# Kernel optimization log

Hardware: AMD Instinct MI355X
Metric: run time of the kernel (lower is better)

## Reference

```python
import jax, jax.numpy as jnp
import numpy as np

HIDDEN = 1024
HEADS = 16
HEAD_DIM = HIDDEN // HEADS


def setup_inputs() -> dict:
    key = jax.random.key(0)
    ks = jax.random.split(key, 8)
    B, S = 2, 2048
    scale = 1.0 / np.sqrt(HIDDEN)
    return {
        "hidden_states": jax.random.normal(ks[0], (B, S, HIDDEN), dtype=jnp.float32),
        "attention_mask": jax.random.randint(ks[1], (B, S), 0, 2, dtype=jnp.int32),
        "Wq": jax.random.normal(ks[2], (HIDDEN, HIDDEN), dtype=jnp.float32) * scale,
        "bq": jax.random.normal(ks[3], (HIDDEN,), dtype=jnp.float32) * 0.02,
        "Wk": jax.random.normal(ks[4], (HIDDEN, HIDDEN), dtype=jnp.float32) * scale,
        "bk": jax.random.normal(ks[5], (HIDDEN,), dtype=jnp.float32) * 0.02,
        "Wv": jax.random.normal(ks[6], (HIDDEN, HIDDEN), dtype=jnp.float32) * scale,
        "bv": jax.random.normal(ks[7], (HIDDEN,), dtype=jnp.float32) * 0.02,
    }


def _split_heads(x):
    # [B, S, H*D] -> [B, H, S, D]
    B, S, _ = x.shape
    return x.reshape(B, S, HEADS, HEAD_DIM).transpose(0, 2, 1, 3)


def reference(hidden_states, attention_mask, Wq, bq, Wk, bk, Wv, bv):
    B, S, _ = hidden_states.shape
    q = _split_heads(hidden_states @ Wq + bq) / jnp.sqrt(jnp.asarray(HEAD_DIM, hidden_states.dtype))
    k = _split_heads(hidden_states @ Wk + bk)
    v = _split_heads(hidden_states @ Wv + bv)
    # scores: [B, H, S, S]
    scores = jnp.einsum("bhqd,bhkd->bhqk", q, k).astype(jnp.float32)
    mask = attention_mask[:, None, None, :]  # [B,1,1,S]
    scores = jnp.where(mask == 0, jnp.float32(-1e8), scores)
    probs = jax.nn.softmax(scores, axis=-1).astype(v.dtype)
    ctx = jnp.einsum("bhqk,bhkd->bhqd", probs, v)
    return ctx.transpose(0, 2, 1, 3).reshape(B, S, HIDDEN)
```

## Files before the change

kernel.cpp:

```cpp
#include <hip/hip_runtime.h>
#include <math.h>

typedef __attribute__((ext_vector_type(4))) float f32x4;
typedef __attribute__((ext_vector_type(16))) float f32x16;
typedef _Float16 f16x8 __attribute__((ext_vector_type(8)));
typedef __fp16 fp16x2 __attribute__((ext_vector_type(2)));
typedef unsigned int uintv2 __attribute__((ext_vector_type(2)));

#define MFMA16(a, b, c) __builtin_amdgcn_mfma_f32_16x16x32_f16((a), (b), (c), 0, 0, 0)
#define MFMA32(a, b, c) __builtin_amdgcn_mfma_f32_32x32x16_f16((a), (b), (c), 0, 0, 0)

__device__ __forceinline__ unsigned short f2h(float f) {
    union { _Float16 h; unsigned short u; } v; v.h = (_Float16)f; return v.u;
}
__device__ __forceinline__ unsigned pk2f(float a, float b) {
    union { fp16x2 h; unsigned u; } v; v.h = __builtin_amdgcn_cvt_pkrtz(a, b); return v.u;
}

#if defined(__has_builtin)
#if __has_builtin(__builtin_amdgcn_global_load_lds)
#define HAVE_GLL 1
#endif
#endif

__device__ __forceinline__ void gload16(const void* g, void* lds) {
#ifdef HAVE_GLL
    __builtin_amdgcn_global_load_lds(
        (const __attribute__((address_space(1))) void*)g,
        (__attribute__((address_space(3))) void*)lds, 16, 0, 0);
#else
    *(f16x8*)lds = *(const f16x8*)g;
#endif
}

__global__ __launch_bounds__(256) void prep_kernel(
    const float* __restrict__ X, const float* __restrict__ Wq,
    const float* __restrict__ Wk, const float* __restrict__ Wv,
    const int* __restrict__ mask,
    unsigned short* __restrict__ XF, unsigned short* __restrict__ WT,
    int* __restrict__ sel, int* __restrict__ kept,
    float* __restrict__ cmask_c) {
    __shared__ float T[64][65];
    __shared__ int wsum[4];
    __shared__ int ktot;
    const int bid = blockIdx.x, t = threadIdx.x;
    if (bid < 4096) {
        int i = (bid * 256 + t) * 4;
        float4 v = *reinterpret_cast<const float4*>(X + i);
        ushort4 h;
        h.x = f2h(v.x); h.y = f2h(v.y); h.z = f2h(v.z); h.w = f2h(v.w);
        *reinterpret_cast<ushort4*>(XF + i) = h;
        return;
    }
    if (bid >= 4864) {
        const int b = bid - 4864;
        const int lane = t & 63, wv = t >> 6;
        const int i0 = b * 2048 + t * 8;
        int mv[8];
        {
            int4 ma = *reinterpret_cast<const int4*>(mask + i0);
            int4 mb = *reinterpret_cast<const int4*>(mask + i0 + 4);
            mv[0] = ma.x != 0; mv[1] = ma.y != 0; mv[2] = ma.z != 0; mv[3] = ma.w != 0;
            mv[4] = mb.x != 0; mv[5] = mb.y != 0; mv[6] = mb.z != 0; mv[7] = mb.w != 0;
        }
        int s = 0;
#pragma unroll
        for (int j = 0; j < 8; ++j) s += mv[j];
        int v = s;
#pragma unroll
        for (int off = 1; off < 64; off <<= 1) {
            int o = __shfl_up(v, off);
            if (lane >= off) v += o;
        }
        if (lane == 63) wsum[wv] = v;
        __syncthreads();
        int woff = 0;
        for (int i = 0; i < wv; ++i) woff += wsum[i];
        const int incl = v + woff;
        int p = incl - s;
#pragma unroll
        for (int j = 0; j < 8; ++j) {
            if (mv[j]) sel[b * 2048 + p] = t * 8 + j;
            p += mv[j];
        }
        if (t == 255) { ktot = incl; kept[b] = incl; }
        __syncthreads();
        const int kt = ktot;
#pragma unroll
        for (int j = 0; j < 8; ++j)
            cmask_c[i0 + j] = (t * 8 + j < kt) ? -13.f : -1e9f;
        return;
    }
    const int t2 = bid - 4096;
    const int z = t2 >> 8, rem = t2 & 255;
    const int k0 = (rem & 15) * 64, n0 = (rem >> 4) * 64;
    const float* W = (z == 0) ? Wq : ((z == 1) ? Wk : Wv);
    unsigned short* Wo = WT + (size_t)z * 1024 * 1024;
    for (int i = 0; i < 4; i++) {
        int fid = t + i * 256;
        int rr = fid >> 4, cc = fid & 15;
        float4 v = *reinterpret_cast<const float4*>(W + (size_t)(k0 + rr) * 1024 + n0 + cc * 4);
        T[rr][cc * 4 + 0] = v.x; T[rr][cc * 4 + 1] = v.y;
        T[rr][cc * 4 + 2] = v.z; T[rr][cc * 4 + 3] = v.w;
    }
    __syncthreads();
    for (int i = 0; i < 4; i++) {
        int e = t + i * 256;
        int n = e >> 4, kq = (e & 15) * 4;
        ushort4 h;
        h.x = f2h(T[kq + 0][n]); h.y = f2h(T[kq + 1][n]);
        h.z = f2h(T[kq + 2][n]); h.w = f2h(T[kq + 3][n]);
        size_t o = (size_t)(n0 + n) * 1024 + k0 + kq;
        *reinterpret_cast<ushort4*>(Wo + o) = h;
    }
}

__global__ __launch_bounds__(256) void gather_xc_kernel(
    const unsigned short* __restrict__ XF, const int* __restrict__ sel,
    const int* __restrict__ kept, unsigned short* __restrict__ XC) {
    const int x = blockIdx.x, t = threadIdx.x;
    const int b = x >> 11, j = x & 2047;
    if (j >= kept[b]) return;
    const int s = sel[b * 2048 + j];
    const unsigned short* src = XF + ((size_t)b * 2048 + s) * 1024;
    unsigned short* dst = XC + ((size_t)b * 2048 + j) * 1024;
    *reinterpret_cast<ushort4*>(dst + t * 4) =
        *reinterpret_cast<const ushort4*>(src + t * 4);
}

__global__ __launch_bounds__(256, 3) void qkv_gemm_kernel(
    const unsigned short* __restrict__ XF, const unsigned short* __restrict__ XC,
    const unsigned short* __restrict__ WT,
    const float* __restrict__ bq, const float* __restrict__ bk,
    const float* __restrict__ bv, const int* __restrict__ kept,
    unsigned short* __restrict__ QF, unsigned short* __restrict__ KC,
    unsigned short* __restrict__ VC) {
    __shared__ __align__(16) char smem[3][2][8192];
    const int z = blockIdx.z;
    const unsigned short* Wz = WT + (size_t)z * 1024 * 1024;
    const float* bias = (z == 0) ? bq : ((z == 1) ? bk : bv);
    const int n0 = blockIdx.y * 128;
    int bb = 0, mb0;
    const unsigned short* Xs;
    if (z == 0) {
        mb0 = blockIdx.x * 128;
        Xs = XF;
    } else {
        bb = blockIdx.x >> 4;
        mb0 = (blockIdx.x & 15) * 128;
        const int kneed = (kept[bb] + 63) & ~63;
        if (mb0 >= kneed) return;
        Xs = XC + (size_t)bb * 2048 * 1024;
    }
    const int tid = threadIdx.x, lane = tid & 63, wid = tid >> 6;
    const int wr = wid >> 1, wc = wid & 1;
    const int g = lane >> 4, r16 = lane & 15;

    f32x4 acc[4][4] = {};

#define QSTAGE(BUFI, K0)                                                             \
    {                                                                                \
        _Pragma("unroll")                                                            \
        for (int p = 0; p < 2; ++p) {                                                \
            int row = p * 64 + (tid >> 2);                                           \
            int ec = ((tid & 3) ^ (row & 3)) * 8;                                    \
            size_t xo = (size_t)(mb0 + row) * 1024 + (K0) + ec;                      \
            size_t wo = (size_t)(n0 + row) * 1024 + (K0) + ec;                       \
            gload16(Xs + xo, &smem[(BUFI)][0][0] + p * 4096 + tid * 16);             \
            gload16(Wz + wo, &smem[(BUFI)][1][0] + p * 4096 + tid * 16);             \
        }                                                                            \
    }

    QSTAGE(0, 0);
    QSTAGE(1, 32);
    int bufc = 0, bufs = 2;
    for (int ki = 0; ki < 32; ++ki) {
        if (ki < 31) {
            asm volatile("s_waitcnt vmcnt(4)" ::: "memory");
        } else {
            asm volatile("s_waitcnt vmcnt(0)" ::: "memory");
        }
        __builtin_amdgcn_s_barrier();
        if (ki < 30) QSTAGE(bufs, (ki + 2) * 32);
        const char* bX = &smem[bufc][0][0];
        const char* bW = &smem[bufc][1][0];
        const int sx = (r16 & 3) << 4;

        f16x8 af[4], bf[4];
#pragma unroll
        for (int mi = 0; mi < 4; ++mi)
            af[mi] = *(const f16x8*)(bX + (wr * 64 + mi * 16 + r16) * 64 + ((g << 4) ^ sx));
#pragma unroll
        for (int ni = 0; ni < 4; ++ni)
            bf[ni] = *(const f16x8*)(bW + (wc * 64 + ni * 16 + r16) * 64 + ((g << 4) ^ sx));
        __builtin_amdgcn_s_setprio(1);
#pragma unroll
        for (int mi = 0; mi < 4; ++mi)
#pragma unroll
            for (int ni = 0; ni < 4; ++ni)
                acc[mi][ni] = MFMA16(af[mi], bf[ni], acc[mi][ni]);
        __builtin_amdgcn_s_setprio(0);
        bufc = (bufc == 2) ? 0 : bufc + 1;
        bufs = (bufs == 2) ? 0 : bufs + 1;
    }

#pragma unroll
    for (int mi = 0; mi < 4; ++mi)
#pragma unroll
        for (int ni = 0; ni < 4; ++ni)
#pragma unroll
            for (int r = 0; r < 4; ++r) {
                int m = mb0 + wr * 64 + mi * 16 + g * 4 + r;
                int n = n0 + wc * 64 + ni * 16 + r16;
                float val = acc[mi][ni][r] + bias[n];
                if (z == 0) val *= 0.18033688011112042f;
                int hh = n >> 6, d = n & 63;
                unsigned short hv = f2h(val);
                if (z == 0) {
                    int b = m >> 11, s = m & 2047;
                    QF[((size_t)(b * 16 + hh) * 2048 + s) * 64 + d] = hv;
                } else if (z == 1) {
                    KC[((size_t)(bb * 16 + hh) * 2048 + m) * 64 + d] = hv;
                } else {
                    VC[((size_t)(bb * 16 + hh) * 64 + d) * 2048 + m] = hv;
                }
            }
}

__global__ __launch_bounds__(256, 4) void attn_kernel(
    const unsigned short* __restrict__ QF, const unsigned short* __restrict__ KC,
    const unsigned short* __restrict__ VC, const float* __restrict__ cmask_c,
    const int* __restrict__ kept, float* __restrict__ out) {
    __shared__ __align__(16) char smem[2][2][8192];
    __shared__ __align__(16) float cmlds[2048];
    const int tid = threadIdx.x;
    const int lane = tid & 63, wid = tid >> 6;
    const int hi = lane >> 5, l31 = lane & 31;
    const int bid = blockIdx.x;
    const int wgid = (bid & 7) * 128 + (bid >> 3);
    const int bh = wgid >> 5, qb = wgid & 31;
    const int b = bh >> 4, h = bh & 15;
    const int qh = wid & 1, kh = wid >> 1;
    const size_t base = (size_t)bh * 2048 * 64;
    const unsigned short* KFh = KC + base;
    const unsigned short* VTh = VC + base;
    const int qrow = qb * 64 + qh * 32 + l31;
    const int swz = (l31 & 7) << 4;
    const int kt = kept[b];
    const int nch = (kt + 63) >> 6;

    f16x8 qf[4];
#pragma unroll
    for (int ks = 0; ks < 4; ++ks)
        qf[ks] = *reinterpret_cast<const f16x8*>(QF + base + (size_t)qrow * 64 + ks * 16 + hi * 8);

    const int lr = lane >> 3, c16 = lane & 7;
    const int gce = (c16 ^ lr) << 3;
    const int pl = wid >> 1, half = wid & 1;
    const unsigned short* mys = pl ? VTh : KFh;
    const int rstr = pl ? 2048 : 64;

    f32x16 ctx[2] = {};
    float l_st = 0.f;

#define STAGE(BUFI, K0)                                                              \
    {                                                                                \
        char* dst = &smem[(BUFI)][pl][0] + half * 4096;                              \
        size_t koff = pl ? (size_t)(K0) : (size_t)(K0) * 64;                         \
        _Pragma("unroll")                                                            \
        for (int i = 0; i < 4; ++i) {                                                \
            int r = half * 32 + i * 8 + lr;                                          \
            gload16(mys + koff + (size_t)r * rstr + gce, dst + i * 1024 + lane * 16);\
        }                                                                            \
    }

    STAGE(0, 0);
    {
        float4 c0 = *reinterpret_cast<const float4*>(cmask_c + b * 2048 + tid * 8);
        float4 c1 = *reinterpret_cast<const float4*>(cmask_c + b * 2048 + tid * 8 + 4);
        *reinterpret_cast<float4*>(&cmlds[tid * 8]) = c0;
        *reinterpret_cast<float4*>(&cmlds[tid * 8 + 4]) = c1;
    }

    for (int ch = 0; ch < nch; ++ch) {
        asm volatile("s_waitcnt vmcnt(0) lgkmcnt(0)" ::: "memory");
        __builtin_amdgcn_s_barrier();
        if (ch + 1 < nch) STAGE((ch + 1) & 1, (ch + 1) * 64);
        const int buf = ch & 1;
        const char* bK = &smem[buf][0][0];
        const char* bV = &smem[buf][1][0];
        const int k0s = ch * 64 + kh * 32;

        f32x16 sc;
        {
            const char* rK = bK + (kh * 32 + l31) * 128;
            f32x16 a = {};
            __builtin_amdgcn_s_setprio(1);
#pragma unroll
            for (int ks = 0; ks < 4; ++ks)
                a = MFMA32(*(const f16x8*)(rK + ((ks * 32 + hi * 16) ^ swz)), qf[ks], a);
            __builtin_amdgcn_s_setprio(0);
            sc = a;
        }

        float p[16];
        float psum = 0.f;
#pragma unroll
        for (int G = 0; G < 4; ++G) {
            float4 cv = *reinterpret_cast<const float4*>(&cmlds[k0s + 8 * G + 4 * hi]);
            int bo = G * 4;
            float e0 = __builtin_amdgcn_exp2f(sc[bo + 0] + cv.x);
            float e1 = __builtin_amdgcn_exp2f(sc[bo + 1] + cv.y);
            float e2 = __builtin_amdgcn_exp2f(sc[bo + 2] + cv.z);
            float e3 = __builtin_amdgcn_exp2f(sc[bo + 3] + cv.w);
            p[bo + 0] = e0; p[bo + 1] = e1; p[bo + 2] = e2; p[bo + 3] = e3;
            psum += e0 + e1 + e2 + e3;
        }
        l_st += psum;

        f16x8 pf[2];
        {
            unsigned a0 = pk2f(p[0], p[1]),   a1 = pk2f(p[2], p[3]);
            unsigned b0 = pk2f(p[4], p[5]),   b1 = pk2f(p[6], p[7]);
            unsigned c0 = pk2f(p[8], p[9]),   c1 = pk2f(p[10], p[11]);
            unsigned d0 = pk2f(p[12], p[13]), d1 = pk2f(p[14], p[15]);
            uintv2 r0 = __builtin_amdgcn_permlane32_swap(a0, b0, false, false);
            uintv2 r1 = __builtin_amdgcn_permlane32_swap(a1, b1, false, false);
            uintv2 r2 = __builtin_amdgcn_permlane32_swap(c0, d0, false, false);
            uintv2 r3 = __builtin_amdgcn_permlane32_swap(c1, d1, false, false);
            union { unsigned u[4]; f16x8 v; } f0, f1;
            f0.u[0] = r0[0]; f0.u[1] = r1[0]; f0.u[2] = r0[1]; f0.u[3] = r1[1];
            f1.u[0] = r2[0]; f1.u[1] = r3[0]; f1.u[2] = r2[1]; f1.u[3] = r3[1];
            pf[0] = f0.v; pf[1] = f1.v;
        }

        __builtin_amdgcn_s_setprio(1);
#pragma unroll
        for (int dt = 0; dt < 2; ++dt) {
            const char* rV = bV + (dt * 32 + l31) * 128;
            f32x16 a = ctx[dt];
#pragma unroll
            for (int ks = 0; ks < 2; ++ks)
                a = MFMA32(*(const f16x8*)(rV + ((kh * 64 + ks * 32 + hi * 16) ^ swz)), pf[ks], a);
            ctx[dt] = a;
        }
        __builtin_amdgcn_s_setprio(0);
    }

    l_st += __shfl_xor(l_st, 32);
    asm volatile("s_waitcnt lgkmcnt(0)" ::: "memory");
    __builtin_amdgcn_s_barrier();
    float* scr = (float*)&smem[0][0][0];
    if (kh) {
        float* dst = scr + qh * 2304 + lane * 36;
#pragma unroll
        for (int dt = 0; dt < 2; ++dt)
#pragma unroll
            for (int G = 0; G < 4; ++G) {
                float4 st;
                st.x = ctx[dt][G * 4 + 0]; st.y = ctx[dt][G * 4 + 1];
                st.z = ctx[dt][G * 4 + 2]; st.w = ctx[dt][G * 4 + 3];
                *reinterpret_cast<float4*>(dst + dt * 16 + G * 4) = st;
            }
        scr[4608 + qh * 64 + lane] = l_st;
        asm volatile("s_waitcnt lgkmcnt(0)" ::: "memory");
    }
    __builtin_amdgcn_s_barrier();
    if (!kh) {
        const float* src = scr + qh * 2304 + lane * 36;
        float l_full = l_st + scr[4608 + qh * 64 + lane];
        float inv_l = 1.0f / l_full;
        size_t ob0 = ((size_t)b * 2048 + qrow) * 1024 + h * 64 + 4 * hi;
#pragma unroll
        for (int dt = 0; dt < 2; ++dt)
#pragma unroll
            for (int G = 0; G < 4; ++G) {
                float4 pv = *reinterpret_cast<const float4*>(src + dt * 16 + G * 4);
                float4 st;
                st.x = (ctx[dt][G * 4 + 0] + pv.x) * inv_l;
                st.y = (ctx[dt][G * 4 + 1] + pv.y) * inv_l;
                st.z = (ctx[dt][G * 4 + 2] + pv.z) * inv_l;
                st.w = (ctx[dt][G * 4 + 3] + pv.w) * inv_l;
                *reinterpret_cast<float4*>(out + ob0 + dt * 32 + 8 * G) = st;
            }
    }
}

extern "C" void kernel_launch(void* const* d_in, const int* in_sizes, int n_in,
                              void* d_out, int out_size, void* d_ws, size_t ws_size,
                              hipStream_t stream) {
    const float* X  = (const float*)d_in[0];
    const int* mask = (const int*)d_in[1];
    const float* Wq = (const float*)d_in[2];
    const float* bq = (const float*)d_in[3];
    const float* Wk = (const float*)d_in[4];
    const float* bk = (const float*)d_in[5];
    const float* Wv = (const float*)d_in[6];
    const float* bv = (const float*)d_in[7];
    float* out = (float*)d_out;

    char* ws = (char*)d_ws;
    const size_t SZ_X = (size_t)4096 * 1024 * 2;
    const size_t SZ_W = (size_t)1024 * 1024 * 2;
    const size_t SZ_Q = (size_t)2 * 16 * 2048 * 64 * 2;
    unsigned short* XF = (unsigned short*)(ws);
    unsigned short* WT = (unsigned short*)(ws + SZ_X);
    unsigned short* QF = (unsigned short*)(ws + SZ_X + 3 * SZ_W);
    unsigned short* KC = (unsigned short*)(ws + SZ_X + 3 * SZ_W + 1 * SZ_Q);
    unsigned short* VC = (unsigned short*)(ws + SZ_X + 3 * SZ_W + 2 * SZ_Q);
    unsigned short* XC = (unsigned short*)(ws + SZ_X + 3 * SZ_W + 3 * SZ_Q);
    char* extra = ws + SZ_X + 3 * SZ_W + 4 * SZ_Q;
    int* SEL    = (int*)(extra);
    int* KEPT   = (int*)(extra + 16384);
    float* CMC  = (float*)(extra + 16384 + 256);

    prep_kernel<<<4866, 256, 0, stream>>>(X, Wq, Wk, Wv, mask, XF, WT, SEL, KEPT, CMC);
    gather_xc_kernel<<<4096, 256, 0, stream>>>(XF, SEL, KEPT, XC);
    qkv_gemm_kernel<<<dim3(32, 8, 3), 256, 0, stream>>>(XF, XC, WT, bq, bk, bv, KEPT,
                                                        QF, KC, VC);
    attn_kernel<<<1024, 256, 0, stream>>>(QF, KC, VC, CMC, KEPT, out);
}
```

Baseline: 89.93 us.

## Fuse kept-row gather into QKV GEMM loads and remap blocks for XCD locality

Removes the separate gather kernel that copied kept rows of X into a compacted buffer. The GEMM now reads rows of XF directly through per-thread row pointers taken from the selection index. Padding entries of sel are zeroed so out-of-range rows read a valid location. The grid becomes 1D, and blocks are laid out so that each XCD (block index mod 8) owns one N-column slice, which should improve L2 reuse of weights. The cost is indirect row addresses in the GEMM loads, which may coalesce less well.

```diff
diff --git a/kernel.cpp b/kernel.cpp
--- a/kernel.cpp
+++ b/kernel.cpp
@@ -87,8 +87,11 @@
         __syncthreads();
         const int kt = ktot;
 #pragma unroll
-        for (int j = 0; j < 8; ++j)
-            cmask_c[i0 + j] = (t * 8 + j < kt) ? -13.f : -1e9f;
+        for (int j = 0; j < 8; ++j) {
+            int idx = t * 8 + j;
+            cmask_c[b * 2048 + idx] = (idx < kt) ? -13.f : -1e9f;
+            if (idx >= kt) sel[b * 2048 + idx] = 0;
+        }
         return;
     }
     const int t2 = bid - 4096;
@@ -115,46 +118,47 @@
     }
 }
 
-__global__ __launch_bounds__(256) void gather_xc_kernel(
-    const unsigned short* __restrict__ XF, const int* __restrict__ sel,
-    const int* __restrict__ kept, unsigned short* __restrict__ XC) {
-    const int x = blockIdx.x, t = threadIdx.x;
-    const int b = x >> 11, j = x & 2047;
-    if (j >= kept[b]) return;
-    const int s = sel[b * 2048 + j];
-    const unsigned short* src = XF + ((size_t)b * 2048 + s) * 1024;
-    unsigned short* dst = XC + ((size_t)b * 2048 + j) * 1024;
-    *reinterpret_cast<ushort4*>(dst + t * 4) =
-        *reinterpret_cast<const ushort4*>(src + t * 4);
-}
-
 __global__ __launch_bounds__(256, 3) void qkv_gemm_kernel(
-    const unsigned short* __restrict__ XF, const unsigned short* __restrict__ XC,
-    const unsigned short* __restrict__ WT,
+    const unsigned short* __restrict__ XF, const unsigned short* __restrict__ WT,
     const float* __restrict__ bq, const float* __restrict__ bk,
-    const float* __restrict__ bv, const int* __restrict__ kept,
+    const float* __restrict__ bv, const int* __restrict__ sel,
+    const int* __restrict__ kept,
     unsigned short* __restrict__ QF, unsigned short* __restrict__ KC,
     unsigned short* __restrict__ VC) {
     __shared__ __align__(16) char smem[3][2][8192];
-    const int z = blockIdx.z;
+    const int bid = blockIdx.x;
+    const int xcd = bid & 7, ii = bid >> 3;
+    const int z = ii % 3, xb = ii / 3;
+    const int n0 = xcd * 128;
     const unsigned short* Wz = WT + (size_t)z * 1024 * 1024;
     const float* bias = (z == 0) ? bq : ((z == 1) ? bk : bv);
-    const int n0 = blockIdx.y * 128;
     int bb = 0, mb0;
-    const unsigned short* Xs;
     if (z == 0) {
-        mb0 = blockIdx.x * 128;
-        Xs = XF;
+        mb0 = xb * 128;
     } else {
-        bb = blockIdx.x >> 4;
-        mb0 = (blockIdx.x & 15) * 128;
-        const int kneed = (kept[bb] + 63) & ~63;
-        if (mb0 >= kneed) return;
-        Xs = XC + (size_t)bb * 2048 * 1024;
+        bb = xb >> 4;
+        mb0 = (xb & 15) * 128;
+        if (mb0 >= ((kept[bb] + 63) & ~63)) return;
     }
     const int tid = threadIdx.x, lane = tid & 63, wid = tid >> 6;
     const int wr = wid >> 1, wc = wid & 1;
     const int g = lane >> 4, r16 = lane & 15;
+
+    const int r0 = tid >> 2;
+    const int ec = ((tid & 3) ^ (r0 & 3)) * 8;
+    const unsigned short* xbase[2];
+    const unsigned short* wbase[2];
+#pragma unroll
+    for (int p = 0; p < 2; ++p) {
+        int row = p * 64 + r0;
+        if (z == 0) {
+            xbase[p] = XF + (size_t)(mb0 + row) * 1024 + ec;
+        } else {
+            int src = sel[bb * 2048 + mb0 + row];
+            xbase[p] = XF + ((size_t)bb * 2048 + src) * 1024 + ec;
+        }
+        wbase[p] = Wz + (size_t)(n0 + row) * 1024 + ec;
+    }
 
     f32x4 acc[4][4] = {};
 
@@ -162,12 +166,8 @@
     {                                                                                \
         _Pragma("unroll")                                                            \
         for (int p = 0; p < 2; ++p) {                                                \
-            int row = p * 64 + (tid >> 2);                                           \
-            int ec = ((tid & 3) ^ (row & 3)) * 8;                                    \
-            size_t xo = (size_t)(mb0 + row) * 1024 + (K0) + ec;                      \
-            size_t wo = (size_t)(n0 + row) * 1024 + (K0) + ec;                       \
-            gload16(Xs + xo, &smem[(BUFI)][0][0] + p * 4096 + tid * 16);             \
-            gload16(Wz + wo, &smem[(BUFI)][1][0] + p * 4096 + tid * 16);             \
+            gload16(xbase[p] + (K0), &smem[(BUFI)][0][0] + p * 4096 + tid * 16);     \
+            gload16(wbase[p] + (K0), &smem[(BUFI)][1][0] + p * 4096 + tid * 16);     \
         }                                                                            \
     }
 
@@ -408,15 +408,12 @@
     unsigned short* QF = (unsigned short*)(ws + SZ_X + 3 * SZ_W);
     unsigned short* KC = (unsigned short*)(ws + SZ_X + 3 * SZ_W + 1 * SZ_Q);
     unsigned short* VC = (unsigned short*)(ws + SZ_X + 3 * SZ_W + 2 * SZ_Q);
-    unsigned short* XC = (unsigned short*)(ws + SZ_X + 3 * SZ_W + 3 * SZ_Q);
-    char* extra = ws + SZ_X + 3 * SZ_W + 4 * SZ_Q;
+    char* extra = ws + SZ_X + 3 * SZ_W + 3 * SZ_Q;
     int* SEL    = (int*)(extra);
     int* KEPT   = (int*)(extra + 16384);
     float* CMC  = (float*)(extra + 16384 + 256);
 
     prep_kernel<<<4866, 256, 0, stream>>>(X, Wq, Wk, Wv, mask, XF, WT, SEL, KEPT, CMC);
-    gather_xc_kernel<<<4096, 256, 0, stream>>>(XF, SEL, KEPT, XC);
-    qkv_gemm_kernel<<<dim3(32, 8, 3), 256, 0, stream>>>(XF, XC, WT, bq, bk, bv, KEPT,
-                                                        QF, KC, VC);
+    qkv_gemm_kernel<<<768, 256, 0, stream>>>(XF, WT, bq, bk, bv, SEL, KEPT, QF, KC, VC);
     attn_kernel<<<1024, 256, 0, stream>>>(QF, KC, VC, CMC, KEPT, out);
 }
```

Result: faster. 86.51 us (median of 2 runs) (-3.8%).
